# Kernel optimization log

Measured on AMD Instinct MI355X. Metric: run time of the kernel, lower is better.

The kernel has to match this reference:

```python
import jax, jax.numpy as jnp
import numpy as np

B, S, D, H = 2, 4096, 1024, 16
DH = D // H            # head dim = 64
W = 256                # one-sided attention window (attention_window // 2)
NC = S // W            # number of query chunks
NEG = -1e9


def setup_inputs() -> dict:
    key = jax.random.key(0)
    ks = jax.random.split(key, 8)
    sc = 0.02
    return {
        "hidden_states": jax.random.normal(ks[0], (B, S, D), jnp.float32),
        # additive float mask: 0 = local token, <0 = padding, >0 = global. All zeros here.
        "attention_mask": jnp.zeros((B, 1, 1, S), jnp.float32),
        "Wq": jax.random.normal(ks[1], (D, D), jnp.float32) * sc,
        "bq": jnp.zeros((D,), jnp.float32),
        "Wk": jax.random.normal(ks[2], (D, D), jnp.float32) * sc,
        "bk": jnp.zeros((D,), jnp.float32),
        "Wv": jax.random.normal(ks[3], (D, D), jnp.float32) * sc,
        "bv": jnp.zeros((D,), jnp.float32),
        "Wo": jax.random.normal(ks[4], (D, D), jnp.float32) * sc,
        "bo": jnp.zeros((D,), jnp.float32),
    }


def _heads(x, w, b):
    # [B,S,D] -> [B,H,S,DH]
    return (x @ w + b).reshape(B, S, H, DH).transpose(0, 2, 1, 3)


def _forward(hidden_states, attention_mask, Wq, bq, Wk, bk, Wv, bv, Wo, bo):
    mask = attention_mask[:, 0, 0, :]                    # [B,S] additive key mask
    q = _heads(hidden_states, Wq, bq) / jnp.sqrt(jnp.float32(DH))
    k = _heads(hidden_states, Wk, bk)
    v = _heads(hidden_states, Wv, bv)

    # Overlapping key/value chunks: chunk c covers padded positions [c*W, c*W+3W),
    # i.e. global keys [c*W - W, c*W + 2W) -- the union of the windows of its W queries.
    idx = jnp.arange(NC)[:, None] * W + jnp.arange(3 * W)[None, :]   # [NC,3W] into padded axis
    k_pad = jnp.pad(k, ((0, 0), (0, 0), (W, W), (0, 0)))
    v_pad = jnp.pad(v, ((0, 0), (0, 0), (W, W), (0, 0)))
    k_ch = k_pad[:, :, idx]                               # [B,H,NC,3W,DH]
    v_ch = v_pad[:, :, idx]                               # [B,H,NC,3W,DH]
    mask_ch = jnp.pad(mask, ((0, 0), (W, W)))[:, idx]     # [B,NC,3W]

    q_ch = q.reshape(B, H, NC, W, DH)
    scores = jnp.einsum('bhcqd,bhckd->bhcqk', q_ch, k_ch)  # [B,H,NC,W,3W]

    # Band mask: query local p attends key local o with 0 <= o - p <= 2W.
    rel = jnp.arange(3 * W)[None, :] - jnp.arange(W)[:, None]        # [W,3W]
    band = (rel >= 0) & (rel <= 2 * W)
    key_gidx = idx - W                                               # global key index
    valid = (key_gidx >= 0) & (key_gidx < S)                         # [NC,3W]
    allowed = band[None, :, :] & valid[:, None, :]                   # [NC,W,3W]

    scores = scores + mask_ch[:, None, :, None, :]
    scores = jnp.where(allowed[None, None], scores, NEG)
    probs = jax.nn.softmax(scores, axis=-1)

    out = jnp.einsum('bhcqk,bhckd->bhcqd', probs, v_ch)    # [B,H,NC,W,DH]
    out = out.reshape(B, H, S, DH).transpose(0, 2, 1, 3).reshape(B, S, D)
    return out @ Wo + bo


def reference(hidden_states, attention_mask, Wq, bq, Wk, bk, Wv, bv, Wo, bo):
    return _forward(hidden_states, attention_mask, Wq, bq, Wk, bk, Wv, bv, Wo, bo)
```

## Files before the change

kernel.cpp:

```cpp
#include <hip/hip_runtime.h>

typedef unsigned short u16;
typedef __bf16 bf16x8 __attribute__((ext_vector_type(8)));
typedef u16 u16x8 __attribute__((ext_vector_type(8)));
typedef float f32x4 __attribute__((ext_vector_type(4)));
typedef unsigned uint2v __attribute__((ext_vector_type(2)));

#define LOG2E 1.4426950408889634f

static __device__ __forceinline__ u16 f2bf(float f) {
    union { float f; unsigned u; } x; x.f = f;
    unsigned r = x.u + 0x7fffu + ((x.u >> 16) & 1u);
    return (u16)(r >> 16);
}

static __device__ __forceinline__ unsigned cvtpk(float lo, float hi) {
    unsigned r;
    asm("v_cvt_pk_bf16_f32 %0, %1, %2" : "=v"(r) : "v"(lo), "v"(hi));
    return r;
}

static __device__ __forceinline__ void gl_lds16(const void* g, void* l) {
    __builtin_amdgcn_global_load_lds(
        (const __attribute__((address_space(1))) void*)g,
        (__attribute__((address_space(3))) void*)l, 16, 0, 0);
}

__global__ __launch_bounds__(256) void cvt_k(const float* __restrict__ src,
                                             u16* __restrict__ dst, int n) {
    int i = (blockIdx.x * 256 + threadIdx.x) * 4;
    if (i < n) {
        float4 v = *(const float4*)(src + i);
        ushort4 o;
        o.x = f2bf(v.x); o.y = f2bf(v.y); o.z = f2bf(v.z); o.w = f2bf(v.w);
        *(ushort4*)(dst + i) = o;
    }
}

__global__ __launch_bounds__(256) void transw_k(const float* __restrict__ w0,
                                                const float* __restrict__ w1,
                                                const float* __restrict__ w2,
                                                const float* __restrict__ w3,
                                                u16* __restrict__ wt) {
    __shared__ float T[64][65];
    const float* src = (blockIdx.z == 0) ? w0 : (blockIdx.z == 1) ? w1
                     : (blockIdx.z == 2) ? w2 : w3;
    u16* dst = wt + (size_t)blockIdx.z * 1048576;
    const int k0 = blockIdx.x * 64, n0 = blockIdx.y * 64;
    const int rr = threadIdx.x >> 6, col = threadIdx.x & 63;
#pragma unroll
    for (int i = 0; i < 16; ++i) {
        int row = i * 4 + rr;
        T[row][col] = src[(size_t)(k0 + row) * 1024 + n0 + col];
    }
    __syncthreads();
#pragma unroll
    for (int i = 0; i < 16; ++i) {
        int row = i * 4 + rr;
        dst[(size_t)(n0 + row) * 1024 + k0 + col] = f2bf(T[col][row]);
    }
}

__global__ __launch_bounds__(256, 2) void gemm_k(
    const u16* __restrict__ A, const u16* __restrict__ WT0,
    const float* __restrict__ b0, const float* __restrict__ b1,
    const float* __restrict__ b2,
    u16* __restrict__ o0, u16* __restrict__ o1, u16* __restrict__ o2,
    float* __restrict__ oF, int mode) {
    __shared__ alignas(16) u16 Al[128 * 32];
    __shared__ alignas(16) u16 Bl[128 * 32];

    const int tid = threadIdx.x;
    const int lane = tid & 63;
    const int wv = tid >> 6;
    const int wr = wv >> 1, wc = wv & 1;
    const int l15 = lane & 15, l4 = lane >> 4;

    const int mbase = blockIdx.x * 128;
    const int sel = blockIdx.y >> 3;
    const int nb = (blockIdx.y & 7) * 128;

    const u16* Ab = A + (size_t)mbase * 1024;
    const u16* Bb = WT0 + (size_t)sel * 1048576 + (size_t)nb * 1024;

    const int srow = tid >> 2;
    const int scol = (tid & 3) * 8;

    f32x4 acc[4][4] = {};

    for (int k0 = 0; k0 < 1024; k0 += 32) {
        char* la = (char*)Al + wv * 1024;
        char* lb = (char*)Bl + wv * 1024;
        gl_lds16(Ab + (size_t)srow * 1024 + k0 + scol, la);
        gl_lds16(Ab + (size_t)(srow + 64) * 1024 + k0 + scol, la + 4096);
        gl_lds16(Bb + (size_t)srow * 1024 + k0 + scol, lb);
        gl_lds16(Bb + (size_t)(srow + 64) * 1024 + k0 + scol, lb + 4096);
        __syncthreads();

        bf16x8 af[4], bfr[4];
#pragma unroll
        for (int mr = 0; mr < 4; ++mr)
            af[mr] = *(const bf16x8*)(Al + (wr * 64 + mr * 16 + l15) * 32 + l4 * 8);
#pragma unroll
        for (int nr = 0; nr < 4; ++nr)
            bfr[nr] = *(const bf16x8*)(Bl + (wc * 64 + nr * 16 + l15) * 32 + l4 * 8);
#pragma unroll
        for (int mr = 0; mr < 4; ++mr)
#pragma unroll
            for (int nr = 0; nr < 4; ++nr)
                acc[mr][nr] = __builtin_amdgcn_mfma_f32_16x16x32_bf16(
                    af[mr], bfr[nr], acc[mr][nr], 0, 0, 0);
        __syncthreads();
    }

    const float* bias = (sel == 0) ? b0 : ((sel == 1) ? b1 : b2);
    u16* oH = (sel == 0) ? o0 : ((sel == 1) ? o1 : o2);
    const float scale = (mode == 0 && sel == 0) ? 0.125f * LOG2E : 1.0f;

#pragma unroll
    for (int mr = 0; mr < 4; ++mr)
#pragma unroll
        for (int nr = 0; nr < 4; ++nr) {
            int col = nb + wc * 64 + nr * 16 + l15;
            float bv_ = bias[col];
#pragma unroll
            for (int j = 0; j < 4; ++j) {
                int row = mbase + wr * 64 + mr * 16 + l4 * 4 + j;
                float v = (acc[mr][nr][j] + bv_) * scale;
                if (mode == 0) {
                    int b_ = row >> 12, s_ = row & 4095;
                    int h_ = col >> 6, d_ = col & 63;
                    oH[(((size_t)(b_ * 16 + h_) * 4096) + s_) * 64 + d_] = f2bf(v);
                } else {
                    oF[(size_t)row * 1024 + col] = v;
                }
            }
        }
}

__global__ __launch_bounds__(256, 4) void attn_k(
    const u16* __restrict__ Qh, const u16* __restrict__ Kh,
    const u16* __restrict__ Vh, const float* __restrict__ mask,
    u16* __restrict__ attnb) {
    __shared__ alignas(16) u16 Kt[2][4096];
    __shared__ alignas(16) u16 Vt[4096];
    __shared__ alignas(16) u16 Pl[4][1024];
    __shared__ alignas(16) float maskl[640];

    const int tid = threadIdx.x;
    const int lane = tid & 63;
    const int wv = tid >> 6;
    const int hw = blockIdx.x;
    const int lg = (hw & 7) * 128 + (hw >> 3);
    const int c = lg & 31;
    const int h = (lg >> 5) & 15;
    const int b = lg >> 9;

    const size_t bh = (size_t)(b * 16 + h) * 4096;
    const u16* Qb = Qh + bh * 64;
    const u16* Kb = Kh + bh * 64;
    const u16* Vb = Vh + bh * 64;
    const float* mb = mask + b * 4096;

    const int l15 = lane & 15;
    const int l4 = lane >> 4;
    const int qbase = c * 128 + wv * 32;
    const int gkbase = c * 128 - 256;

    bf16x8 qf[2][2];
#pragma unroll
    for (int qt = 0; qt < 2; ++qt)
#pragma unroll
        for (int kc = 0; kc < 2; ++kc)
            qf[qt][kc] = *(const bf16x8*)(Qb + (size_t)(qbase + qt * 16 + l15) * 64 + kc * 32 + l4 * 8);

    f32x4 Ov[4][2] = {};
    float lsum[2] = {0.f, 0.f};
    float m[2] = {-3.0e38f, -3.0e38f};

    const int kslot = lane & 7;
    const int krow8 = lane >> 3;
    const int vrow = tid >> 3;
    const int vd0 = (tid & 7) * 8;

    const int tmin = wv >> 1;
    const int tmax_t = 8 + (wv >> 1);

    {
#pragma unroll
        for (int i = 0; i < 2; ++i) {
            int row = i * 32 + wv * 8 + krow8;
            int key = min(max(gkbase + row, 0), 4095);
            gl_lds16(Kb + (size_t)key * 64 + ((kslot ^ (row & 7)) * 8),
                     &Kt[0][(i * 32 + wv * 8) * 64]);
        }
#pragma unroll
        for (int i = 0; i < 2; ++i) {
            int vk = i * 32 + vrow;
            int key = min(max(gkbase + vk, 0), 4095);
            u16x8 vv = *(const u16x8*)(Vb + (size_t)key * 64 + vd0);
            int vbx = (vk >> 3) ^ (tid & 7);
#pragma unroll
            for (int e = 0; e < 8; ++e)
                Vt[(vd0 + e) * 64 + ((vbx ^ e) * 8) + (vk & 7)] = vv[e];
        }
        for (int i = tid; i < 640; i += 256) {
            int gm = gkbase + i;
            maskl[i] = (gm >= 0 && gm < 4096) ? mb[gm] * LOG2E : 0.f;
        }
    }
    __syncthreads();

    for (int t = 0; t < 10; ++t) {
        const int cur = t & 1, nxt = cur ^ 1;
        const int gk0 = gkbase + t * 64;
        const bool pre = (t < 9);

        u16x8 vv[2] = {};
        if (pre) {
            const int gk0n = gk0 + 64;
#pragma unroll
            for (int i = 0; i < 2; ++i) {
                int row = i * 32 + wv * 8 + krow8;
                int key = min(max(gk0n + row, 0), 4095);
                gl_lds16(Kb + (size_t)key * 64 + ((kslot ^ (row & 7)) * 8),
                         &Kt[nxt][(i * 32 + wv * 8) * 64]);
            }
#pragma unroll
            for (int i = 0; i < 2; ++i) {
                int key = min(max(gk0n + i * 32 + vrow, 0), 4095);
                vv[i] = *(const u16x8*)(Vb + (size_t)key * 64 + vd0);
            }
        }

        if (t >= tmin && t <= tmax_t) {
            f32x4 mv[4];
#pragma unroll
            for (int kb = 0; kb < 4; ++kb)
                mv[kb] = *(const f32x4*)(maskl + t * 64 + kb * 16 + l4 * 4);

            f32x4 sc[4][2] = {};
            __builtin_amdgcn_s_setprio(1);
#pragma unroll
            for (int kc = 0; kc < 2; ++kc)
#pragma unroll
                for (int kb = 0; kb < 4; ++kb) {
                    int r = kb * 16 + l15;
                    bf16x8 kf = *(const bf16x8*)(&Kt[cur][r * 64 + (((kc * 4 + l4) ^ (r & 7)) * 8)]);
                    sc[kb][0] = __builtin_amdgcn_mfma_f32_16x16x32_bf16(kf, qf[0][kc], sc[kb][0], 0, 0, 0);
                    sc[kb][1] = __builtin_amdgcn_mfma_f32_16x16x32_bf16(kf, qf[1][kc], sc[kb][1], 0, 0, 0);
                }
            __builtin_amdgcn_s_setprio(0);

            const int kb0 = gk0 + l4 * 4;
            const int ub0 = kb0 - (qbase + l15) + 256;
#pragma unroll
            for (int kb = 0; kb < 4; ++kb)
#pragma unroll
                for (int qt = 0; qt < 2; ++qt)
#pragma unroll
                    for (int j = 0; j < 4; ++j) {
                        float sv = sc[kb][qt][j] + mv[kb][j];
                        unsigned band = (unsigned)(ub0 + kb * 16 + j - qt * 16);
                        unsigned keyv = (unsigned)(kb0 + kb * 16 + j);
                        bool ok = (band <= 512u) && (keyv < 4096u);
                        sc[kb][qt][j] = ok ? sv : -3.0e9f;
                    }

            u16* Pw = &Pl[wv][0];
            const int prow = l15 * 64;
#pragma unroll
            for (int qt = 0; qt < 2; ++qt) {
                float mx = sc[0][qt][0];
#pragma unroll
                for (int kb = 0; kb < 4; ++kb)
#pragma unroll
                    for (int j = 0; j < 4; ++j) mx = fmaxf(mx, sc[kb][qt][j]);
                mx = fmaxf(mx, __shfl_xor(mx, 16));
                mx = fmaxf(mx, __shfl_xor(mx, 32));
                float mnew = fmaxf(m[qt], mx);
                float alpha = exp2f(m[qt] - mnew);
                m[qt] = mnew;
                lsum[qt] *= alpha;
#pragma unroll
                for (int nd = 0; nd < 4; ++nd) Ov[nd][qt] *= alpha;

                float s0 = 0.f;
#pragma unroll
                for (int kb = 0; kb < 4; ++kb) {
                    float p0 = exp2f(sc[kb][qt][0] - mnew);
                    float p1 = exp2f(sc[kb][qt][1] - mnew);
                    float p2 = exp2f(sc[kb][qt][2] - mnew);
                    float p3 = exp2f(sc[kb][qt][3] - mnew);
                    s0 += (p0 + p1) + (p2 + p3);
                    uint2v pk;
                    pk[0] = cvtpk(p0, p1);
                    pk[1] = cvtpk(p2, p3);
                    int g = (((kb * 2 + (l4 >> 1)) ^ (l15 & 7)) * 8) + (l4 & 1) * 4;
                    *(uint2v*)(Pw + prow + g) = pk;
                }
                lsum[qt] += s0;

#pragma unroll
                for (int kc = 0; kc < 2; ++kc) {
                    bf16x8 pf = *(const bf16x8*)(Pw + prow + (((kc * 4 + l4) ^ (l15 & 7)) * 8));
                    __builtin_amdgcn_s_setprio(1);
#pragma unroll
                    for (int nd = 0; nd < 4; ++nd) {
                        int r2 = nd * 16 + l15;
                        bf16x8 vf = *(const bf16x8*)(&Vt[r2 * 64 +
                            (((kc * 4 + l4) ^ (r2 & 7) ^ ((r2 >> 3) & 7)) * 8)]);
                        Ov[nd][qt] = __builtin_amdgcn_mfma_f32_16x16x32_bf16(vf, pf, Ov[nd][qt], 0, 0, 0);
                    }
                    __builtin_amdgcn_s_setprio(0);
                }
            }
        }

        __syncthreads();
        if (pre) {
#pragma unroll
            for (int i = 0; i < 2; ++i) {
                int vk = i * 32 + vrow;
                int vbx = (vk >> 3) ^ (tid & 7);
#pragma unroll
                for (int e = 0; e < 8; ++e)
                    Vt[(vd0 + e) * 64 + ((vbx ^ e) * 8) + (vk & 7)] = vv[i][e];
            }
        }
        __syncthreads();
    }

    lsum[0] += __shfl_xor(lsum[0], 16);
    lsum[0] += __shfl_xor(lsum[0], 32);
    lsum[1] += __shfl_xor(lsum[1], 16);
    lsum[1] += __shfl_xor(lsum[1], 32);
    float inv0 = 1.0f / lsum[0];
    float inv1 = 1.0f / lsum[1];
#pragma unroll
    for (int qt = 0; qt < 2; ++qt) {
        float inv = qt ? inv1 : inv0;
        size_t rowb = ((size_t)b * 4096 + qbase + qt * 16 + l15) * 1024 + h * 64 + l4 * 4;
#pragma unroll
        for (int nd = 0; nd < 4; ++nd) {
            uint2v o;
            o[0] = cvtpk(Ov[nd][qt][0] * inv, Ov[nd][qt][1] * inv);
            o[1] = cvtpk(Ov[nd][qt][2] * inv, Ov[nd][qt][3] * inv);
            *(uint2v*)(&attnb[rowb + nd * 16]) = o;
        }
    }
}

extern "C" void kernel_launch(void* const* d_in, const int* in_sizes, int n_in,
                              void* d_out, int out_size, void* d_ws, size_t ws_size,
                              hipStream_t stream) {
    (void)in_sizes; (void)n_in; (void)out_size; (void)ws_size;
    const float* hid  = (const float*)d_in[0];
    const float* mask = (const float*)d_in[1];
    const float* Wq = (const float*)d_in[2];
    const float* bq = (const float*)d_in[3];
    const float* Wk = (const float*)d_in[4];
    const float* bk = (const float*)d_in[5];
    const float* Wv = (const float*)d_in[6];
    const float* bv = (const float*)d_in[7];
    const float* Wo = (const float*)d_in[8];
    const float* bo = (const float*)d_in[9];
    float* out = (float*)d_out;

    char* ws = (char*)d_ws;
    u16* hidb  = (u16*)(ws);
    u16* wt    = (u16*)(ws + (16u << 20));
    u16* Qh    = (u16*)(ws + (24u << 20));
    u16* Kh    = (u16*)(ws + (40u << 20));
    u16* Vh    = (u16*)(ws + (56u << 20));
    u16* attnb = (u16*)(ws + (72u << 20));

    cvt_k<<<dim3(8192), dim3(256), 0, stream>>>(hid, hidb, 8388608);
    transw_k<<<dim3(16, 16, 4), dim3(256), 0, stream>>>(Wq, Wk, Wv, Wo, wt);
    gemm_k<<<dim3(64, 24), dim3(256), 0, stream>>>(hidb, wt, bq, bk, bv,
                                                   Qh, Kh, Vh, (float*)nullptr, 0);
    attn_k<<<dim3(1024), dim3(256), 0, stream>>>(Qh, Kh, Vh, mask, attnb);
    gemm_k<<<dim3(64, 8), dim3(256), 0, stream>>>(attnb, wt + 3 * 1048576, bo, bo, bo,
                                                  (u16*)nullptr, (u16*)nullptr, (u16*)nullptr,
                                                  out, 1);
}
```

Before: 203.2 us.

## Load K fragments directly from global into registers and double-buffer V in LDS

K is no longer staged through LDS via global_load_lds. Each wave now loads its K MFMA fragments straight from global memory into registers inside the compute branch. V becomes double-buffered in LDS, which removes one __syncthreads per iteration. Launch bounds drop to 3 waves/SIMD occupancy, giving more registers. The trade-off: K global loads now sit on the critical path with no prefetch, and neighbouring waves fetch the same K rows redundantly, served from cache instead of shared LDS.

```diff
diff --git a/kernel.cpp b/kernel.cpp
--- a/kernel.cpp
+++ b/kernel.cpp
@@ -138,12 +138,11 @@
         }
 }
 
-__global__ __launch_bounds__(256, 4) void attn_k(
+__global__ __launch_bounds__(256, 3) void attn_k(
     const u16* __restrict__ Qh, const u16* __restrict__ Kh,
     const u16* __restrict__ Vh, const float* __restrict__ mask,
     u16* __restrict__ attnb) {
-    __shared__ alignas(16) u16 Kt[2][4096];
-    __shared__ alignas(16) u16 Vt[4096];
+    __shared__ alignas(16) u16 Vt[2][4096];
     __shared__ alignas(16) u16 Pl[4][1024];
     __shared__ alignas(16) float maskl[640];
 
@@ -178,22 +177,13 @@
     float lsum[2] = {0.f, 0.f};
     float m[2] = {-3.0e38f, -3.0e38f};
 
-    const int kslot = lane & 7;
-    const int krow8 = lane >> 3;
     const int vrow = tid >> 3;
     const int vd0 = (tid & 7) * 8;
 
     const int tmin = wv >> 1;
-    const int tmax_t = 8 + (wv >> 1);
+    const int tmaxw = 8 + (wv >> 1);
 
     {
-#pragma unroll
-        for (int i = 0; i < 2; ++i) {
-            int row = i * 32 + wv * 8 + krow8;
-            int key = min(max(gkbase + row, 0), 4095);
-            gl_lds16(Kb + (size_t)key * 64 + ((kslot ^ (row & 7)) * 8),
-                     &Kt[0][(i * 32 + wv * 8) * 64]);
-        }
 #pragma unroll
         for (int i = 0; i < 2; ++i) {
             int vk = i * 32 + vrow;
@@ -202,7 +192,7 @@
             int vbx = (vk >> 3) ^ (tid & 7);
 #pragma unroll
             for (int e = 0; e < 8; ++e)
-                Vt[(vd0 + e) * 64 + ((vbx ^ e) * 8) + (vk & 7)] = vv[e];
+                Vt[0][(vd0 + e) * 64 + ((vbx ^ e) * 8) + (vk & 7)] = vv[e];
         }
         for (int i = tid; i < 640; i += 256) {
             int gm = gkbase + i;
@@ -221,19 +211,21 @@
             const int gk0n = gk0 + 64;
 #pragma unroll
             for (int i = 0; i < 2; ++i) {
-                int row = i * 32 + wv * 8 + krow8;
-                int key = min(max(gk0n + row, 0), 4095);
-                gl_lds16(Kb + (size_t)key * 64 + ((kslot ^ (row & 7)) * 8),
-                         &Kt[nxt][(i * 32 + wv * 8) * 64]);
-            }
-#pragma unroll
-            for (int i = 0; i < 2; ++i) {
                 int key = min(max(gk0n + i * 32 + vrow, 0), 4095);
                 vv[i] = *(const u16x8*)(Vb + (size_t)key * 64 + vd0);
             }
         }
 
-        if (t >= tmin && t <= tmax_t) {
+        if (t >= tmin && t <= tmaxw) {
+            bf16x8 kfr[2][4];
+#pragma unroll
+            for (int kc = 0; kc < 2; ++kc)
+#pragma unroll
+                for (int kb = 0; kb < 4; ++kb) {
+                    int key = min(max(gk0 + kb * 16 + l15, 0), 4095);
+                    kfr[kc][kb] = *(const bf16x8*)(Kb + (size_t)key * 64 + kc * 32 + l4 * 8);
+                }
+
             f32x4 mv[4];
 #pragma unroll
             for (int kb = 0; kb < 4; ++kb)
@@ -245,10 +237,8 @@
             for (int kc = 0; kc < 2; ++kc)
 #pragma unroll
                 for (int kb = 0; kb < 4; ++kb) {
-                    int r = kb * 16 + l15;
-                    bf16x8 kf = *(const bf16x8*)(&Kt[cur][r * 64 + (((kc * 4 + l4) ^ (r & 7)) * 8)]);
-                    sc[kb][0] = __builtin_amdgcn_mfma_f32_16x16x32_bf16(kf, qf[0][kc], sc[kb][0], 0, 0, 0);
-                    sc[kb][1] = __builtin_amdgcn_mfma_f32_16x16x32_bf16(kf, qf[1][kc], sc[kb][1], 0, 0, 0);
+                    sc[kb][0] = __builtin_amdgcn_mfma_f32_16x16x32_bf16(kfr[kc][kb], qf[0][kc], sc[kb][0], 0, 0, 0);
+                    sc[kb][1] = __builtin_amdgcn_mfma_f32_16x16x32_bf16(kfr[kc][kb], qf[1][kc], sc[kb][1], 0, 0, 0);
                 }
             __builtin_amdgcn_s_setprio(0);
 
@@ -308,7 +298,7 @@
 #pragma unroll
                     for (int nd = 0; nd < 4; ++nd) {
                         int r2 = nd * 16 + l15;
-                        bf16x8 vf = *(const bf16x8*)(&Vt[r2 * 64 +
+                        bf16x8 vf = *(const bf16x8*)(&Vt[cur][r2 * 64 +
                             (((kc * 4 + l4) ^ (r2 & 7) ^ ((r2 >> 3) & 7)) * 8)]);
                         Ov[nd][qt] = __builtin_amdgcn_mfma_f32_16x16x32_bf16(vf, pf, Ov[nd][qt], 0, 0, 0);
                     }
@@ -317,7 +307,6 @@
             }
         }
 
-        __syncthreads();
         if (pre) {
 #pragma unroll
             for (int i = 0; i < 2; ++i) {
@@ -325,7 +314,7 @@
                 int vbx = (vk >> 3) ^ (tid & 7);
 #pragma unroll
                 for (int e = 0; e < 8; ++e)
-                    Vt[(vd0 + e) * 64 + ((vbx ^ e) * 8) + (vk & 7)] = vv[i][e];
+                    Vt[nxt][(vd0 + e) * 64 + ((vbx ^ e) * 8) + (vk & 7)] = vv[i][e];
             }
         }
         __syncthreads();
```

Result: faster. 195.6 us (-3.7%).
